# Performance work log

Hardware: AMD Instinct MI355X
Metric: run time of the kernel (lower is better)

Reference implementation:

```python
import jax, jax.numpy as jnp
import numpy as np

B, T, D, H, HD = 2, 2048, 1024, 16, 64


def setup_inputs() -> dict:
    key = jax.random.key(0)
    kx, kq, kk, kv, ko = jax.random.split(key, 5)
    s = 1.0 / np.sqrt(D)
    return {
        "x": jax.random.normal(kx, (B, T, D), dtype=jnp.float32),
        "Wq": jax.random.normal(kq, (H, D, HD), dtype=jnp.float32) * s,
        "Wk": jax.random.normal(kk, (H, D, HD), dtype=jnp.float32) * s,
        "Wv": jax.random.normal(kv, (H, D, HD), dtype=jnp.float32) * s,
        "Wo": jax.random.normal(ko, (D, D), dtype=jnp.float32) * s,
        "bo": jnp.zeros((D,), dtype=jnp.float32),
    }


def reference(x, Wq, Wk, Wv, Wo, bo):
    # Batched equivalent of the per-head loop: q/k/v for all heads at once.
    q = jnp.einsum("btd,hdk->bhtk", x, Wq)  # [B,H,T,HD]
    k = jnp.einsum("btd,hdk->bhtk", x, Wk)
    v = jnp.einsum("btd,hdk->bhtk", x, Wv)
    scale = 1.0 / jnp.sqrt(jnp.asarray(HD, dtype=x.dtype))
    scores = jnp.einsum("bhqk,bhsk->bhqs", q, k) * scale  # [B,H,T,T]
    causal = jnp.tril(jnp.ones((T, T), dtype=bool))
    scores = jnp.where(causal, scores, jnp.asarray(-1e9, dtype=scores.dtype))
    attn = jax.nn.softmax(scores, axis=-1)
    out = jnp.einsum("bhqs,bhsk->bhqk", attn, v)  # [B,H,T,HD]
    out = out.transpose(0, 2, 1, 3).reshape(B, T, H * HD)  # concat heads
    return out @ Wo + bo  # dropout is identity in eval (p used at train only)
```

## Files before the change

### kernel.cpp

```cpp
#include <hip/hip_runtime.h>
#include <hip/hip_bf16.h>
#include <stdint.h>
#include <stddef.h>

typedef __bf16 bf16_t;
typedef __attribute__((ext_vector_type(4))) __bf16 bf16x4;
typedef __attribute__((ext_vector_type(8))) __bf16 bf16x8;
typedef __attribute__((ext_vector_type(4))) float floatx4;

#define GLD16(gp, lp) __builtin_amdgcn_global_load_lds(                      \
    (__attribute__((address_space(1))) void*)(gp),                           \
    (__attribute__((address_space(3))) void*)(lp), 16, 0, 0)

__global__ __launch_bounds__(256) void prep(
    const float* __restrict__ x, const float* __restrict__ Wq,
    const float* __restrict__ Wk, const float* __restrict__ Wv,
    const float* __restrict__ Wo, bf16_t* __restrict__ XB,
    bf16_t* __restrict__ WT, bf16_t* __restrict__ WoT) {
  __shared__ bf16_t t[64][65];
  int bx = blockIdx.x;
  const int tid = threadIdx.x;
  if (bx < 2048) {
    const int i = (bx * 256 + tid) * 8;
    const float4 v0 = *(const float4*)(x + i);
    const float4 v1 = *(const float4*)(x + i + 4);
    bf16x8 o = {(bf16_t)v0.x, (bf16_t)v0.y, (bf16_t)v0.z, (bf16_t)v0.w,
                (bf16_t)v1.x, (bf16_t)v1.y, (bf16_t)v1.z, (bf16_t)v1.w};
    *(bf16x8*)(XB + i) = o;
    return;
  }
  bx -= 2048;
  const int g = tid >> 6, l = tid & 63;
  if (bx < 768) {
    const int d0 = (bx & 15) * 64, h = (bx >> 4) & 15, z = bx >> 8;
    const float* W = (z == 0) ? Wq : (z == 1) ? Wk : Wv;
    const float* src = W + (size_t)h * 65536 + (size_t)d0 * 64;
    #pragma unroll
    for (int i = 0; i < 16; ++i) { int r = g * 16 + i; t[r][l] = (bf16_t)src[(size_t)r * 64 + l]; }
    __syncthreads();
    bf16_t* dst = WT + ((size_t)z * 1024 + h * 64) * 1024 + d0;
    #pragma unroll
    for (int i = 0; i < 16; ++i) { int c = g * 16 + i; dst[(size_t)c * 1024 + l] = t[l][c]; }
  } else {
    bx -= 768;
    const int r0 = (bx & 15) * 64, c0 = (bx >> 4) * 64;
    #pragma unroll
    for (int i = 0; i < 16; ++i) { int r = g * 16 + i; t[r][l] = (bf16_t)Wo[(size_t)(r0 + r) * 1024 + c0 + l]; }
    __syncthreads();
    #pragma unroll
    for (int i = 0; i < 16; ++i) { int c = g * 16 + i; WoT[(size_t)(c0 + c) * 1024 + r0 + l] = t[l][c]; }
  }
}

template <bool BIAS, typename OutT>
__device__ __forceinline__ void gemm_body(
    const bf16_t* __restrict__ A, const bf16_t* __restrict__ Bt,
    OutT* __restrict__ C, const float* __restrict__ bias,
    int K, int lda, int ldb, int ldc, int m0, int n0,
    bf16_t* As, bf16_t* Bs) {
  const int tid = threadIdx.x;
  const int lane = tid & 63, w = tid >> 6;
  const int qd = lane >> 4, ln = lane & 15;
  const int wm = (w & 1) * 64, wn = (w >> 1) * 64;

  const floatx4 z4 = {0.f, 0.f, 0.f, 0.f};
  floatx4 acc[4][4];
  #pragma unroll
  for (int i = 0; i < 4; ++i)
    #pragma unroll
    for (int j = 0; j < 4; ++j) acc[i][j] = z4;

  for (int k0 = 0; k0 < K; k0 += 64) {
    #pragma unroll
    for (int i = 0; i < 4; ++i) {
      const int c = tid + i * 256;
      const int row = c >> 3;
      const int sg = (c & 7) ^ (row & 7);
      GLD16(A + (size_t)(m0 + row) * lda + k0 + sg * 8, As + (size_t)(w * 64 + i * 256) * 8);
      GLD16(Bt + (size_t)(n0 + row) * ldb + k0 + sg * 8, Bs + (size_t)(w * 64 + i * 256) * 8);
    }
    __syncthreads();
    #pragma unroll
    for (int h = 0; h < 2; ++h) {
      bf16x8 af[4], bfr[4];
      #pragma unroll
      for (int t = 0; t < 4; ++t) {
        const int ra = wm + t * 16 + ln;
        const int rb = wn + t * 16 + ln;
        af[t]  = *(const bf16x8*)(As + (size_t)ra * 64 + (((h * 4 + qd) ^ (ra & 7)) * 8));
        bfr[t] = *(const bf16x8*)(Bs + (size_t)rb * 64 + (((h * 4 + qd) ^ (rb & 7)) * 8));
      }
      #pragma unroll
      for (int mt = 0; mt < 4; ++mt)
        #pragma unroll
        for (int nt = 0; nt < 4; ++nt)
          acc[mt][nt] = __builtin_amdgcn_mfma_f32_16x16x32_bf16(af[mt], bfr[nt], acc[mt][nt], 0, 0, 0);
    }
    __syncthreads();
  }

  #pragma unroll
  for (int nt = 0; nt < 4; ++nt) {
    const int col = n0 + wn + nt * 16 + ln;
    const float bv = BIAS ? bias[col] : 0.f;
    #pragma unroll
    for (int mt = 0; mt < 4; ++mt) {
      const int row = m0 + wm + mt * 16 + qd * 4;
      #pragma unroll
      for (int r = 0; r < 4; ++r)
        C[(size_t)(row + r) * ldc + col] = (OutT)(acc[mt][nt][r] + bv);
    }
  }
}

__global__ __launch_bounds__(256) void proj_gemm(
    const bf16_t* __restrict__ XB, const bf16_t* __restrict__ WT,
    bf16_t* __restrict__ C1, bf16_t* __restrict__ VT) {
  __shared__ __align__(16) bf16_t As[128 * 64];
  __shared__ __align__(16) bf16_t Bs[128 * 64];
  int bx = blockIdx.x;
  if (bx < 512) {
    gemm_body<false, bf16_t>(XB, WT, C1, nullptr, 1024, 1024, 1024, 2048,
                             (bx & 31) * 128, (bx >> 5) * 128, As, Bs);
  } else {
    bx -= 512;
    gemm_body<false, bf16_t>(WT + (size_t)2048 * 1024, XB, VT, nullptr,
                             1024, 1024, 1024, 4096,
                             (bx & 7) * 128, (bx >> 3) * 128, As, Bs);
  }
}

__global__ __launch_bounds__(256) void out_gemm(
    const bf16_t* __restrict__ AO, const bf16_t* __restrict__ WoT,
    float* __restrict__ C, const float* __restrict__ bias) {
  __shared__ __align__(16) bf16_t As[128 * 64];
  __shared__ __align__(16) bf16_t Bs[128 * 64];
  gemm_body<true, float>(AO, WoT, C, bias, 1024, 1024, 1024, 1024,
                         blockIdx.x * 128, blockIdx.y * 128, As, Bs);
}

__global__ __launch_bounds__(256) void flash_attn(
    const bf16_t* __restrict__ C1, const bf16_t* __restrict__ VT,
    bf16_t* __restrict__ AO) {
  constexpr int LDK = 72;
  __shared__ __align__(16) bf16_t Ks[2][64 * LDK];
  __shared__ __align__(16) bf16_t Vs[2][64 * LDK];
  __shared__ __align__(16) bf16_t Ps[4][16 * LDK];
  const int qta = blockIdx.x, qtb = 31 - (int)blockIdx.x;
  const int h = blockIdx.y, b = blockIdx.z;
  const int tid = threadIdx.x, lane = tid & 63, w = tid >> 6;
  const int qd = lane >> 4, ln = lane & 15;
  const bf16_t* Qb = C1 + (size_t)b * 2048 * 2048;

  bf16x8 qa0, qa1, qb0, qb1;
  {
    const bf16_t* qp = Qb + (size_t)(qta * 64 + w * 16 + ln) * 2048 + h * 64 + qd * 8;
    qa0 = *(const bf16x8*)qp;
    qa1 = *(const bf16x8*)(qp + 32);
    qp = Qb + (size_t)(qtb * 64 + w * 16 + ln) * 2048 + h * 64 + qd * 8;
    qb0 = *(const bf16x8*)qp;
    qb1 = *(const bf16x8*)(qp + 32);
  }
  float lsum_a = 0.f, lsum_b = 0.f;
  const floatx4 z4 = {0.f, 0.f, 0.f, 0.f};
  floatx4 oacc_a[4], oacc_b[4];
  #pragma unroll
  for (int t = 0; t < 4; ++t) { oacc_a[t] = z4; oacc_b[t] = z4; }

  const bf16_t* Kg = Qb + 1024 + h * 64;
  const bf16_t* Vg = VT + (size_t)(h * 64) * 4096 + b * 2048;
  const float SCL = 0.18033688011112042f;

  const int c0 = tid, c1 = tid + 256;
  const int r0s = c0 >> 3, s0s = (c0 & 7) * 8;
  const int r1s = c1 >> 3, s1s = (c1 & 7) * 8;

  bf16x8 kr0, kr1, vr0, vr1;
  {
    kr0 = *(const bf16x8*)(Kg + (size_t)r0s * 2048 + s0s);
    kr1 = *(const bf16x8*)(Kg + (size_t)r1s * 2048 + s1s);
    vr0 = *(const bf16x8*)(Vg + (size_t)r0s * 4096 + s0s);
    vr1 = *(const bf16x8*)(Vg + (size_t)r1s * 4096 + s1s);
    *(bf16x8*)(&Ks[0][r0s * LDK + s0s]) = kr0;
    *(bf16x8*)(&Ks[0][r1s * LDK + s1s]) = kr1;
    *(bf16x8*)(&Vs[0][r0s * LDK + s0s]) = vr0;
    *(bf16x8*)(&Vs[0][r1s * LDK + s1s]) = vr1;
  }
  __syncthreads();

  for (int st = 0; st <= qtb; ++st) {
    const int bi = st & 1;
    const bool doA = (st <= qta);
    if (st < qtb) {
      const int s0 = (st + 1) * 64;
      kr0 = *(const bf16x8*)(Kg + (size_t)(s0 + r0s) * 2048 + s0s);
      kr1 = *(const bf16x8*)(Kg + (size_t)(s0 + r1s) * 2048 + s1s);
      vr0 = *(const bf16x8*)(Vg + (size_t)r0s * 4096 + s0 + s0s);
      vr1 = *(const bf16x8*)(Vg + (size_t)r1s * 4096 + s0 + s1s);
    }

    floatx4 sa[4], sb[4];
    #pragma unroll
    for (int nt = 0; nt < 4; ++nt) {
      const bf16_t* kp = &Ks[bi][(nt * 16 + ln) * LDK + qd * 8];
      bf16x8 kf0 = *(const bf16x8*)kp;
      bf16x8 kf1 = *(const bf16x8*)(kp + 32);
      floatx4 t0 = z4;
      t0 = __builtin_amdgcn_mfma_f32_16x16x32_bf16(kf0, qb0, t0, 0, 0, 0);
      t0 = __builtin_amdgcn_mfma_f32_16x16x32_bf16(kf1, qb1, t0, 0, 0, 0);
      sb[nt] = t0;
      if (doA) {
        floatx4 t1 = z4;
        t1 = __builtin_amdgcn_mfma_f32_16x16x32_bf16(kf0, qa0, t1, 0, 0, 0);
        t1 = __builtin_amdgcn_mfma_f32_16x16x32_bf16(kf1, qa1, t1, 0, 0, 0);
        sa[nt] = t1;
      }
    }

    {
      float rs = 0.f;
      #pragma unroll
      for (int nt = 0; nt < 4; ++nt) {
        float p[4];
        #pragma unroll
        for (int r = 0; r < 4; ++r) {
          float v = sb[nt][r] * SCL;
          if (st == qtb && (nt * 16 + qd * 4 + r) > (w * 16 + ln)) v = -1e30f;
          p[r] = __builtin_amdgcn_exp2f(v);
          rs += p[r];
        }
        bf16x4 pk = {(bf16_t)p[0], (bf16_t)p[1], (bf16_t)p[2], (bf16_t)p[3]};
        *(bf16x4*)(&Ps[w][ln * LDK + nt * 16 + qd * 4]) = pk;
      }
      rs += __shfl_xor(rs, 16);
      rs += __shfl_xor(rs, 32);
      lsum_b += rs;
    }
    bf16x8 pb0 = *(const bf16x8*)(&Ps[w][ln * LDK + qd * 8]);
    bf16x8 pb1 = *(const bf16x8*)(&Ps[w][ln * LDK + 32 + qd * 8]);

    bf16x8 pa0, pa1;
    if (doA) {
      float rs = 0.f;
      #pragma unroll
      for (int nt = 0; nt < 4; ++nt) {
        float p[4];
        #pragma unroll
        for (int r = 0; r < 4; ++r) {
          float v = sa[nt][r] * SCL;
          if (st == qta && (nt * 16 + qd * 4 + r) > (w * 16 + ln)) v = -1e30f;
          p[r] = __builtin_amdgcn_exp2f(v);
          rs += p[r];
        }
        bf16x4 pk = {(bf16_t)p[0], (bf16_t)p[1], (bf16_t)p[2], (bf16_t)p[3]};
        *(bf16x4*)(&Ps[w][ln * LDK + nt * 16 + qd * 4]) = pk;
      }
      rs += __shfl_xor(rs, 16);
      rs += __shfl_xor(rs, 32);
      lsum_a += rs;
      pa0 = *(const bf16x8*)(&Ps[w][ln * LDK + qd * 8]);
      pa1 = *(const bf16x8*)(&Ps[w][ln * LDK + 32 + qd * 8]);
    }

    #pragma unroll
    for (int t = 0; t < 4; ++t) {
      const bf16_t* vp = &Vs[bi][(t * 16 + ln) * LDK + qd * 8];
      bf16x8 vf0 = *(const bf16x8*)vp;
      bf16x8 vf1 = *(const bf16x8*)(vp + 32);
      oacc_b[t] = __builtin_amdgcn_mfma_f32_16x16x32_bf16(pb0, vf0, oacc_b[t], 0, 0, 0);
      oacc_b[t] = __builtin_amdgcn_mfma_f32_16x16x32_bf16(pb1, vf1, oacc_b[t], 0, 0, 0);
      if (doA) {
        oacc_a[t] = __builtin_amdgcn_mfma_f32_16x16x32_bf16(pa0, vf0, oacc_a[t], 0, 0, 0);
        oacc_a[t] = __builtin_amdgcn_mfma_f32_16x16x32_bf16(pa1, vf1, oacc_a[t], 0, 0, 0);
      }
    }

    if (st < qtb) {
      const int ni = (st + 1) & 1;
      *(bf16x8*)(&Ks[ni][r0s * LDK + s0s]) = kr0;
      *(bf16x8*)(&Ks[ni][r1s * LDK + s1s]) = kr1;
      *(bf16x8*)(&Vs[ni][r0s * LDK + s0s]) = vr0;
      *(bf16x8*)(&Vs[ni][r1s * LDK + s1s]) = vr1;
    }
    __syncthreads();
  }

  const float rla = 1.0f / lsum_a, rlb = 1.0f / lsum_b;
  #pragma unroll
  for (int r = 0; r < 4; ++r) {
    const float la = __shfl(rla, qd * 4 + r);
    const float lb = __shfl(rlb, qd * 4 + r);
    #pragma unroll
    for (int t = 0; t < 4; ++t) {
      const int col = h * 64 + t * 16 + ln;
      const int rowa = b * 2048 + qta * 64 + w * 16 + qd * 4 + r;
      const int rowb = b * 2048 + qtb * 64 + w * 16 + qd * 4 + r;
      AO[(size_t)rowa * 1024 + col] = (bf16_t)(oacc_a[t][r] * la);
      AO[(size_t)rowb * 1024 + col] = (bf16_t)(oacc_b[t][r] * lb);
    }
  }
}

extern "C" void kernel_launch(void* const* d_in, const int* in_sizes, int n_in,
                              void* d_out, int out_size, void* d_ws, size_t ws_size,
                              hipStream_t stream) {
  const float* x  = (const float*)d_in[0];
  const float* Wq = (const float*)d_in[1];
  const float* Wk = (const float*)d_in[2];
  const float* Wv = (const float*)d_in[3];
  const float* Wo = (const float*)d_in[4];
  const float* bo = (const float*)d_in[5];
  float* out = (float*)d_out;

  bf16_t* WT  = (bf16_t*)d_ws;
  bf16_t* WoT = WT + (size_t)3072 * 1024;
  bf16_t* C1  = WoT + (size_t)1024 * 1024;
  bf16_t* AO  = C1 + (size_t)4096 * 2048;
  bf16_t* XB  = (bf16_t*)d_out;
  bf16_t* VT  = XB + (size_t)4096 * 1024;

  prep<<<dim3(3072), 256, 0, stream>>>(x, Wq, Wk, Wv, Wo, XB, WT, WoT);
  proj_gemm<<<dim3(768), 256, 0, stream>>>(XB, WT, C1, VT);
  flash_attn<<<dim3(16, 16, 2), 256, 0, stream>>>(C1, VT, AO);
  out_gemm<<<dim3(32, 8), 256, 0, stream>>>(AO, WoT, out, bo);
}
```

Baseline: 191.5 us.

## Restructure flash attention: one q-tile per block, async LDS loads, swizzled layout

The attention kernel now handles a single 64-row query tile per block instead of a paired short/long tile, and launches 1024 blocks in a balanced ordering. K/V tiles are staged with global_load_lds straight into XOR-swizzled unpadded LDS rather than through registers. The softmax scale is folded into the Wq conversion in prep, and launch bounds request higher occupancy. The aim is lower register pressure, more waves in flight and less copy overhead. The cost is more blocks that each reload K/V, and per-block causal imbalance that the new ordering has to offset.

```diff
diff --git a/kernel.cpp b/kernel.cpp
--- a/kernel.cpp
+++ b/kernel.cpp
@@ -34,9 +34,10 @@
   if (bx < 768) {
     const int d0 = (bx & 15) * 64, h = (bx >> 4) & 15, z = bx >> 8;
     const float* W = (z == 0) ? Wq : (z == 1) ? Wk : Wv;
+    const float scl = (z == 0) ? 0.18033688011112042f : 1.0f;
     const float* src = W + (size_t)h * 65536 + (size_t)d0 * 64;
     #pragma unroll
-    for (int i = 0; i < 16; ++i) { int r = g * 16 + i; t[r][l] = (bf16_t)src[(size_t)r * 64 + l]; }
+    for (int i = 0; i < 16; ++i) { int r = g * 16 + i; t[r][l] = (bf16_t)(src[(size_t)r * 64 + l] * scl); }
     __syncthreads();
     bf16_t* dst = WT + ((size_t)z * 1024 + h * 64) * 1024 + d0;
     #pragma unroll
@@ -139,82 +140,67 @@
                          blockIdx.x * 128, blockIdx.y * 128, As, Bs);
 }
 
-__global__ __launch_bounds__(256) void flash_attn(
+__global__ __launch_bounds__(256, 4) void flash_attn(
     const bf16_t* __restrict__ C1, const bf16_t* __restrict__ VT,
     bf16_t* __restrict__ AO) {
-  constexpr int LDK = 72;
-  __shared__ __align__(16) bf16_t Ks[2][64 * LDK];
-  __shared__ __align__(16) bf16_t Vs[2][64 * LDK];
-  __shared__ __align__(16) bf16_t Ps[4][16 * LDK];
-  const int qta = blockIdx.x, qtb = 31 - (int)blockIdx.x;
-  const int h = blockIdx.y, b = blockIdx.z;
+  __shared__ __align__(16) bf16_t Ks[2][64 * 64];
+  __shared__ __align__(16) bf16_t Vs[2][64 * 64];
+  __shared__ __align__(16) bf16_t Ps[4][16 * 64];
+
+  const int bid = blockIdx.x;
+  const int kk = bid >> 8, c = bid & 255, u = c & 7;
+  const int qt = (kk == 0) ? u : (kk == 1) ? 15 - u : (kk == 2) ? 16 + u : 31 - u;
+  const int h = (c >> 3) & 15, b = c >> 7;
+
   const int tid = threadIdx.x, lane = tid & 63, w = tid >> 6;
   const int qd = lane >> 4, ln = lane & 15;
   const bf16_t* Qb = C1 + (size_t)b * 2048 * 2048;
 
-  bf16x8 qa0, qa1, qb0, qb1;
+  bf16x8 qf0, qf1;
   {
-    const bf16_t* qp = Qb + (size_t)(qta * 64 + w * 16 + ln) * 2048 + h * 64 + qd * 8;
-    qa0 = *(const bf16x8*)qp;
-    qa1 = *(const bf16x8*)(qp + 32);
-    qp = Qb + (size_t)(qtb * 64 + w * 16 + ln) * 2048 + h * 64 + qd * 8;
-    qb0 = *(const bf16x8*)qp;
-    qb1 = *(const bf16x8*)(qp + 32);
-  }
-  float lsum_a = 0.f, lsum_b = 0.f;
+    const bf16_t* qp = Qb + (size_t)(qt * 64 + w * 16 + ln) * 2048 + h * 64 + qd * 8;
+    qf0 = *(const bf16x8*)qp;
+    qf1 = *(const bf16x8*)(qp + 32);
+  }
+  float lsum = 0.f;
   const floatx4 z4 = {0.f, 0.f, 0.f, 0.f};
-  floatx4 oacc_a[4], oacc_b[4];
-  #pragma unroll
-  for (int t = 0; t < 4; ++t) { oacc_a[t] = z4; oacc_b[t] = z4; }
+  floatx4 oacc[4];
+  #pragma unroll
+  for (int t = 0; t < 4; ++t) oacc[t] = z4;
 
   const bf16_t* Kg = Qb + 1024 + h * 64;
   const bf16_t* Vg = VT + (size_t)(h * 64) * 4096 + b * 2048;
-  const float SCL = 0.18033688011112042f;
-
-  const int c0 = tid, c1 = tid + 256;
-  const int r0s = c0 >> 3, s0s = (c0 & 7) * 8;
-  const int r1s = c1 >> 3, s1s = (c1 & 7) * 8;
-
-  bf16x8 kr0, kr1, vr0, vr1;
-  {
-    kr0 = *(const bf16x8*)(Kg + (size_t)r0s * 2048 + s0s);
-    kr1 = *(const bf16x8*)(Kg + (size_t)r1s * 2048 + s1s);
-    vr0 = *(const bf16x8*)(Vg + (size_t)r0s * 4096 + s0s);
-    vr1 = *(const bf16x8*)(Vg + (size_t)r1s * 4096 + s1s);
-    *(bf16x8*)(&Ks[0][r0s * LDK + s0s]) = kr0;
-    *(bf16x8*)(&Ks[0][r1s * LDK + s1s]) = kr1;
-    *(bf16x8*)(&Vs[0][r0s * LDK + s0s]) = vr0;
-    *(bf16x8*)(&Vs[0][r1s * LDK + s1s]) = vr1;
-  }
-  __syncthreads();
-
-  for (int st = 0; st <= qtb; ++st) {
+
+  const int r0 = tid >> 3;
+  const int g0 = ((tid & 7) ^ (r0 & 7)) * 8;
+
+  auto STAGE = [&](int BUF, int SOFF) {
+    GLD16(Kg + (size_t)(SOFF + r0) * 2048 + g0,      &Ks[BUF][w * 512]);
+    GLD16(Kg + (size_t)(SOFF + r0 + 32) * 2048 + g0, &Ks[BUF][w * 512 + 2048]);
+    GLD16(Vg + (size_t)r0 * 4096 + SOFF + g0,        &Vs[BUF][w * 512]);
+    GLD16(Vg + (size_t)(r0 + 32) * 4096 + SOFF + g0, &Vs[BUF][w * 512 + 2048]);
+  };
+
+  STAGE(0, 0);
+
+  const int e2 = (ln & 7) << 1;
+  const int swf = qd ^ (ln & 7);
+
+  for (int st = 0; st <= qt; ++st) {
     const int bi = st & 1;
-    const bool doA = (st <= qta);
-    if (st < qtb) {
-      const int s0 = (st + 1) * 64;
-      kr0 = *(const bf16x8*)(Kg + (size_t)(s0 + r0s) * 2048 + s0s);
-      kr1 = *(const bf16x8*)(Kg + (size_t)(s0 + r1s) * 2048 + s1s);
-      vr0 = *(const bf16x8*)(Vg + (size_t)r0s * 4096 + s0 + s0s);
-      vr1 = *(const bf16x8*)(Vg + (size_t)r1s * 4096 + s0 + s1s);
-    }
-
-    floatx4 sa[4], sb[4];
+    __syncthreads();
+    if (st < qt) STAGE(bi ^ 1, (st + 1) * 64);
+
+    floatx4 sa[4];
     #pragma unroll
     for (int nt = 0; nt < 4; ++nt) {
-      const bf16_t* kp = &Ks[bi][(nt * 16 + ln) * LDK + qd * 8];
-      bf16x8 kf0 = *(const bf16x8*)kp;
-      bf16x8 kf1 = *(const bf16x8*)(kp + 32);
+      const bf16_t* kp = &Ks[bi][(nt * 16 + ln) * 64];
+      bf16x8 kf0 = *(const bf16x8*)(kp + swf * 8);
+      bf16x8 kf1 = *(const bf16x8*)(kp + (swf ^ 4) * 8);
       floatx4 t0 = z4;
-      t0 = __builtin_amdgcn_mfma_f32_16x16x32_bf16(kf0, qb0, t0, 0, 0, 0);
-      t0 = __builtin_amdgcn_mfma_f32_16x16x32_bf16(kf1, qb1, t0, 0, 0, 0);
-      sb[nt] = t0;
-      if (doA) {
-        floatx4 t1 = z4;
-        t1 = __builtin_amdgcn_mfma_f32_16x16x32_bf16(kf0, qa0, t1, 0, 0, 0);
-        t1 = __builtin_amdgcn_mfma_f32_16x16x32_bf16(kf1, qa1, t1, 0, 0, 0);
-        sa[nt] = t1;
-      }
+      t0 = __builtin_amdgcn_mfma_f32_16x16x32_bf16(kf0, qf0, t0, 0, 0, 0);
+      t0 = __builtin_amdgcn_mfma_f32_16x16x32_bf16(kf1, qf1, t0, 0, 0, 0);
+      sa[nt] = t0;
     }
 
     {
@@ -224,79 +210,40 @@
         float p[4];
         #pragma unroll
         for (int r = 0; r < 4; ++r) {
-          float v = sb[nt][r] * SCL;
-          if (st == qtb && (nt * 16 + qd * 4 + r) > (w * 16 + ln)) v = -1e30f;
+          float v = sa[nt][r];
+          if (st == qt && (nt * 16 + qd * 4 + r) > (w * 16 + ln)) v = -1e30f;
           p[r] = __builtin_amdgcn_exp2f(v);
           rs += p[r];
         }
         bf16x4 pk = {(bf16_t)p[0], (bf16_t)p[1], (bf16_t)p[2], (bf16_t)p[3]};
-        *(bf16x4*)(&Ps[w][ln * LDK + nt * 16 + qd * 4]) = pk;
+        *(bf16x4*)(&Ps[w][ln * 64 + (((nt * 4 + qd) ^ e2) << 2)]) = pk;
       }
       rs += __shfl_xor(rs, 16);
       rs += __shfl_xor(rs, 32);
-      lsum_b += rs;
-    }
-    bf16x8 pb0 = *(const bf16x8*)(&Ps[w][ln * LDK + qd * 8]);
-    bf16x8 pb1 = *(const bf16x8*)(&Ps[w][ln * LDK + 32 + qd * 8]);
-
-    bf16x8 pa0, pa1;
-    if (doA) {
-      float rs = 0.f;
-      #pragma unroll
-      for (int nt = 0; nt < 4; ++nt) {
-        float p[4];
-        #pragma unroll
-        for (int r = 0; r < 4; ++r) {
-          float v = sa[nt][r] * SCL;
-          if (st == qta && (nt * 16 + qd * 4 + r) > (w * 16 + ln)) v = -1e30f;
-          p[r] = __builtin_amdgcn_exp2f(v);
-          rs += p[r];
-        }
-        bf16x4 pk = {(bf16_t)p[0], (bf16_t)p[1], (bf16_t)p[2], (bf16_t)p[3]};
-        *(bf16x4*)(&Ps[w][ln * LDK + nt * 16 + qd * 4]) = pk;
-      }
-      rs += __shfl_xor(rs, 16);
-      rs += __shfl_xor(rs, 32);
-      lsum_a += rs;
-      pa0 = *(const bf16x8*)(&Ps[w][ln * LDK + qd * 8]);
-      pa1 = *(const bf16x8*)(&Ps[w][ln * LDK + 32 + qd * 8]);
-    }
+      lsum += rs;
+    }
+    bf16x8 pa0 = *(const bf16x8*)(&Ps[w][ln * 64 + ((((qd << 1)    ) ^ e2) << 2)]);
+    bf16x8 pa1 = *(const bf16x8*)(&Ps[w][ln * 64 + ((((qd << 1) + 8) ^ e2) << 2)]);
 
     #pragma unroll
     for (int t = 0; t < 4; ++t) {
-      const bf16_t* vp = &Vs[bi][(t * 16 + ln) * LDK + qd * 8];
-      bf16x8 vf0 = *(const bf16x8*)vp;
-      bf16x8 vf1 = *(const bf16x8*)(vp + 32);
-      oacc_b[t] = __builtin_amdgcn_mfma_f32_16x16x32_bf16(pb0, vf0, oacc_b[t], 0, 0, 0);
-      oacc_b[t] = __builtin_amdgcn_mfma_f32_16x16x32_bf16(pb1, vf1, oacc_b[t], 0, 0, 0);
-      if (doA) {
-        oacc_a[t] = __builtin_amdgcn_mfma_f32_16x16x32_bf16(pa0, vf0, oacc_a[t], 0, 0, 0);
-        oacc_a[t] = __builtin_amdgcn_mfma_f32_16x16x32_bf16(pa1, vf1, oacc_a[t], 0, 0, 0);
-      }
-    }
-
-    if (st < qtb) {
-      const int ni = (st + 1) & 1;
-      *(bf16x8*)(&Ks[ni][r0s * LDK + s0s]) = kr0;
-      *(bf16x8*)(&Ks[ni][r1s * LDK + s1s]) = kr1;
-      *(bf16x8*)(&Vs[ni][r0s * LDK + s0s]) = vr0;
-      *(bf16x8*)(&Vs[ni][r1s * LDK + s1s]) = vr1;
-    }
-    __syncthreads();
-  }
-
-  const float rla = 1.0f / lsum_a, rlb = 1.0f / lsum_b;
+      const bf16_t* vp = &Vs[bi][(t * 16 + ln) * 64];
+      bf16x8 vf0 = *(const bf16x8*)(vp + swf * 8);
+      bf16x8 vf1 = *(const bf16x8*)(vp + (swf ^ 4) * 8);
+      oacc[t] = __builtin_amdgcn_mfma_f32_16x16x32_bf16(pa0, vf0, oacc[t], 0, 0, 0);
+      oacc[t] = __builtin_amdgcn_mfma_f32_16x16x32_bf16(pa1, vf1, oacc[t], 0, 0, 0);
+    }
+  }
+
+  const float rl = 1.0f / lsum;
   #pragma unroll
   for (int r = 0; r < 4; ++r) {
-    const float la = __shfl(rla, qd * 4 + r);
-    const float lb = __shfl(rlb, qd * 4 + r);
+    const float lr = __shfl(rl, qd * 4 + r);
     #pragma unroll
     for (int t = 0; t < 4; ++t) {
       const int col = h * 64 + t * 16 + ln;
-      const int rowa = b * 2048 + qta * 64 + w * 16 + qd * 4 + r;
-      const int rowb = b * 2048 + qtb * 64 + w * 16 + qd * 4 + r;
-      AO[(size_t)rowa * 1024 + col] = (bf16_t)(oacc_a[t][r] * la);
-      AO[(size_t)rowb * 1024 + col] = (bf16_t)(oacc_b[t][r] * lb);
+      const int row = b * 2048 + qt * 64 + w * 16 + qd * 4 + r;
+      AO[(size_t)row * 1024 + col] = (bf16_t)(oacc[t][r] * lr);
     }
   }
 }
@@ -321,6 +268,6 @@
 
   prep<<<dim3(3072), 256, 0, stream>>>(x, Wq, Wk, Wv, Wo, XB, WT, WoT);
   proj_gemm<<<dim3(768), 256, 0, stream>>>(XB, WT, C1, VT);
-  flash_attn<<<dim3(16, 16, 2), 256, 0, stream>>>(C1, VT, AO);
+  flash_attn<<<dim3(1024), 256, 0, stream>>>(C1, VT, AO);
   out_gemm<<<dim3(32, 8), 256, 0, stream>>>(AO, WoT, out, bo);
 }
```

Result: faster. 182.2 us (-4.9%).
